# Performance work log

Hardware: AMD Instinct MI355X
Metric: run time of the kernel (lower is better)

## Reference

```python
import jax, jax.numpy as jnp
import numpy as np

NB, NA, NK, NC, NH, NW = 16, 5, 9, 13, 38, 38
MAXT = 50
NUM_LABELS = 2 * NK + 3  # class + 9 (x,y) keypoints + w + h
NOOBJ_SCALE, OBJ_SCALE = 1.0, 5.0
COORD_SCALE, CLASS_SCALE = 1.0, 1.0
SIL_THRESH = 0.6
PRETRAIN_EPOCHS = 15
TH, SHARP, IMW, IMH = 80.0, 2.0, 640.0, 480.0  # utils.corner_confidence defaults


def _corner_conf(dx, dy):
    # dx, dy: pixel-space keypoint deltas, last axis = keypoints
    dist = jnp.sqrt(dx * dx + dy * dy)
    denom = np.exp(SHARP) - 1.0
    c = jnp.where(dist < TH, (jnp.exp(SHARP * (1.0 - dist / TH)) - 1.0) / denom, 0.0)
    return c.mean(axis=-1)


def region_loss(output, target, anchors, epoch):
    nB, _, nH, nW = output.shape
    nA, nK, nC = NA, NK, NC
    out = output.reshape(nB, nA, 2 * nK + 1 + nC, nH, nW)
    x = out[:, :, 0:2 * nK:2]  # (nB,nA,nK,nH,nW)
    y = out[:, :, 1:2 * nK:2]
    x = x.at[:, :, 0].set(jax.nn.sigmoid(x[:, :, 0]))  # only keypoint 0 is sigmoided
    y = y.at[:, :, 0].set(jax.nn.sigmoid(y[:, :, 0]))
    conf = jax.nn.sigmoid(out[:, :, 2 * nK])  # (nB,nA,nH,nW)
    # cls: (nB*nA, nC, nH*nW).transpose(1,2) -> rows ordered (b,a,h,w)
    cls_logits = out[:, :, 2 * nK + 1:].transpose(0, 1, 3, 4, 2).reshape(-1, nC)

    # ---- decoded corners (detached in the original via .data) ----
    gx_grid = jnp.arange(nW, dtype=output.dtype)
    gy_grid = jnp.arange(nH, dtype=output.dtype)[:, None]
    px = jax.lax.stop_gradient((x + gx_grid) / nW)  # (nB,nA,nK,nH,nW)
    py = jax.lax.stop_gradient((y + gy_grid) / nH)
    nAnch = nA * nH * nW
    px_f = px.transpose(0, 1, 3, 4, 2).reshape(nB, nAnch, nK)  # (b, a*h*w, kp)
    py_f = py.transpose(0, 1, 3, 4, 2).reshape(nB, nAnch, nK)

    # ---- build_targets (all constants w.r.t. grads) ----
    tgt = jax.lax.stop_gradient(target).reshape(nB, MAXT, NUM_LABELS)
    gt_x = tgt[:, :, 1:1 + 2 * nK:2]  # (nB,T,nK)
    gt_y = tgt[:, :, 2:2 + 2 * nK:2]
    # loop breaks at first x0 == 0 -> validity is a cumulative product
    valid = jnp.cumprod((gt_x[:, :, 0] != 0).astype(output.dtype), axis=1)  # (nB,T)

    # pass 1: silence anchors already confident for some GT
    dx = (px_f[:, None] - gt_x[:, :, None]) * IMW  # (nB,T,nAnch,nK)
    dy = (py_f[:, None] - gt_y[:, :, None]) * IMH
    confs = _corner_conf(dx, dy) * valid[:, :, None]  # (nB,T,nAnch); invalid->0 == init
    cur_confs = confs.max(axis=1)  # (nB,nAnch)
    conf_mask_flat = jnp.where(cur_confs > SIL_THRESH, 0.0, NOOBJ_SCALE).reshape(-1)

    # pass 2: per-GT assignment
    gi0 = jnp.floor(gt_x[:, :, 0] * nW).astype(jnp.int32)  # (nB,T)
    gj0 = jnp.floor(gt_y[:, :, 0] * nH).astype(jnp.int32)
    gw = tgt[:, :, NUM_LABELS - 2] * nW
    gh = tgt[:, :, NUM_LABELS - 1] * nH
    anc = jax.lax.stop_gradient(anchors).reshape(nA, 2)
    aw, ah = anc[:, 0], anc[:, 1]
    # bbox_iou with both boxes centered at (0,0)
    uw = jnp.maximum(gw[..., None], aw)
    uh = jnp.maximum(gh[..., None], ah)
    cw = gw[..., None] + aw - uw
    ch = gh[..., None] + ah - uh
    carea = cw * ch
    uarea = gw[..., None] * gh[..., None] + aw * ah - carea
    iou = jnp.where((cw > 0) & (ch > 0), carea / uarea, 0.0)  # (nB,T,nA)
    best_n = jnp.argmax(iou, axis=-1)  # (nB,T)

    # faithful to the original bug: pred_box fetched with best_n == -1 (wraps)
    nPix = nH * nW
    pxa = px_f.reshape(nB * nAnch, nK)
    pya = py_f.reshape(nB * nAnch, nK)
    pidx = (jnp.arange(nB)[:, None] * nAnch - nPix + gj0 * nW + gi0) % (nB * nAnch)
    dxx = (gt_x - pxa[pidx]) * IMW  # (nB,T,nK)
    dyy = (gt_y - pya[pidx]) * IMH
    tconf_vals = _corner_conf(dxx, dyy)  # (nB,T)

    Ntot = nB * nA * nH * nW
    flat = ((jnp.arange(nB)[:, None] * nA + best_n) * nH + gj0) * nW + gi0
    flat = jnp.where(valid > 0, flat, Ntot).reshape(-1)  # invalid -> dummy slot

    coord_mask = jnp.zeros(Ntot + 1, output.dtype).at[flat].set(1.0)[:-1]
    cls_mask = coord_mask
    conf_mask = jnp.concatenate([conf_mask_flat, jnp.zeros(1, output.dtype)]).at[flat].set(OBJ_SCALE)[:-1]
    vx = (gt_x * nW - gi0[..., None].astype(output.dtype)).reshape(-1, nK)
    vy = (gt_y * nH - gj0[..., None].astype(output.dtype)).reshape(-1, nK)
    txs = jnp.zeros((Ntot + 1, nK), output.dtype).at[flat].set(vx)[:-1]
    tys = jnp.zeros((Ntot + 1, nK), output.dtype).at[flat].set(vy)[:-1]
    tconf = jnp.zeros(Ntot + 1, output.dtype).at[flat].set(tconf_vals.reshape(-1))[:-1]
    tcls = jnp.zeros(Ntot + 1, output.dtype).at[flat].set(tgt[:, :, 0].reshape(-1))[:-1]

    # ---- losses ----
    cm = coord_mask.reshape(nB, nA, nH, nW)[..., None]
    x_p = x.transpose(0, 1, 3, 4, 2)  # (nB,nA,nH,nW,nK)
    y_p = y.transpose(0, 1, 3, 4, 2)
    loss_x = COORD_SCALE * 0.5 * jnp.sum(((x_p - txs.reshape(nB, nA, nH, nW, nK)) * cm) ** 2)
    loss_y = COORD_SCALE * 0.5 * jnp.sum(((y_p - tys.reshape(nB, nA, nH, nW, nK)) * cm) ** 2)
    sqcm = jnp.sqrt(conf_mask).reshape(nB, nA, nH, nW)
    loss_conf = 0.5 * jnp.sum(((conf - tconf.reshape(nB, nA, nH, nW)) * sqcm) ** 2)
    labels = jnp.clip(tcls.astype(jnp.int32), 0, nC - 1)
    logp = jax.nn.log_softmax(cls_logits, axis=-1)
    ce = -jnp.take_along_axis(logp, labels[:, None], axis=-1)[:, 0]
    loss_cls = CLASS_SCALE * jnp.sum(cls_mask * ce)
    loss = loss_x + loss_y + loss_cls
    if epoch > PRETRAIN_EPOCHS:
        loss = loss + loss_conf
    return loss


def setup_inputs() -> dict:
    key = jax.random.key(0)
    k1, k2, k3, k4, k5 = jax.random.split(key, 5)
    output = jax.random.normal(k1, (NB, NA * (2 * NK + 1 + NC), NH, NW), jnp.float32)
    kp = jax.random.uniform(k2, (NB, MAXT, NK, 2), jnp.float32, 0.05, 0.95)
    wh = jax.random.uniform(k3, (NB, MAXT, 2), jnp.float32, 0.05, 0.5)
    cls = jax.random.randint(k4, (NB, MAXT), 0, NC).astype(jnp.float32)
    nvalid = jax.random.randint(k5, (NB,), 1, 9)
    valid = (jnp.arange(MAXT)[None, :] < nvalid[:, None]).astype(jnp.float32)
    tgt = jnp.concatenate([cls[..., None], kp.reshape(NB, MAXT, 2 * NK), wh], axis=-1)
    target = (tgt * valid[..., None]).reshape(NB, MAXT * NUM_LABELS)
    anchors = jnp.array([1.08, 1.19, 3.42, 4.41, 6.63, 11.38, 9.42, 5.11, 16.62, 10.52], jnp.float32)
    return {"output": output, "target": target, "anchors": anchors, "epoch": 20}


def reference(output, target, anchors, epoch):
    return region_loss(output, target, anchors, epoch)
```

## Files before the change

### kernel.cpp

```cpp
#include <hip/hip_runtime.h>
#include <math.h>

#define NB 16
#define NA 5
#define NK 9
#define NC 13
#define NH 38
#define NW 38
#define MAXT 50
#define NUM_LABELS 21
#define NPIX (NH*NW)
#define NANCH (NA*NPIX)
#define NTOT (NB*NANCH)
#define CHTOT (2*NK+1+NC)

#define TH_F 80.0f
#define SHARP_F 2.0f
#define IMW_F 640.0f
#define IMH_F 480.0f
#define SIL_F 0.6f
#define OBJ_SCALE_F 5.0f
#define NOOBJ_SCALE_F 1.0f
#define PRETRAIN_EPOCHS 15
#define INV_DENOM 0.15651764274966565f

__device__ __forceinline__ float sigmoidf(float v) {
    return 1.0f / (1.0f + __expf(-v));
}

__global__ void prep_kernel(const float* __restrict__ out,
                            const float* __restrict__ tgt,
                            const float* __restrict__ anchors,
                            float* __restrict__ tdata,
                            int* __restrict__ flatidx,
                            int* __restrict__ nvalid,
                            float* __restrict__ d_out)
{
    const int b = blockIdx.x;
    const int t = threadIdx.x;
    __shared__ int nv_s;
    if (t == 0) {
        int nv = 0;
        for (int tt = 0; tt < MAXT; tt++) {
            if (tgt[(long)b * MAXT * NUM_LABELS + tt * NUM_LABELS + 1] != 0.0f) nv++;
            else break;
        }
        nv_s = nv;
        nvalid[b] = nv;
        if (b == 0) d_out[0] = 0.0f;
    }
    __syncthreads();
    const int nv = nv_s;
    if (t >= MAXT) return;
    if (t >= nv) { flatidx[b * MAXT + t] = -1; return; }

    const float* tp = tgt + (long)b * MAXT * NUM_LABELS + t * NUM_LABELS;
    float gx[NK], gy[NK];
#pragma unroll
    for (int k = 0; k < NK; k++) {
        gx[k] = tp[1 + 2 * k];
        gy[k] = tp[2 + 2 * k];
    }
    const int gi0 = (int)floorf(gx[0] * (float)NW);
    const int gj0 = (int)floorf(gy[0] * (float)NH);
    const float gw = tp[NUM_LABELS - 2] * (float)NW;
    const float gh = tp[NUM_LABELS - 1] * (float)NH;

    int best_n = 0;
    float best_iou = -1.0f;
#pragma unroll
    for (int a = 0; a < NA; a++) {
        const float aw = anchors[2 * a], ah = anchors[2 * a + 1];
        const float uw = fmaxf(gw, aw), uh = fmaxf(gh, ah);
        const float cw = gw + aw - uw, ch = gh + ah - uh;
        const float carea = cw * ch;
        const float uarea = gw * gh + aw * ah - carea;
        const float iou = (cw > 0.0f && ch > 0.0f) ? (carea / uarea) : 0.0f;
        if (iou > best_iou) { best_iou = iou; best_n = a; }
    }

    long p = (long)b * NANCH - NPIX + gj0 * NW + gi0;
    p %= (long)NTOT;
    if (p < 0) p += NTOT;
    const int bb  = (int)(p / NANCH);
    const int rem = (int)(p % NANCH);
    const int aa  = rem / NPIX;
    const int pix = rem % NPIX;
    const int jj  = pix / NW;
    const int ii  = pix % NW;

    const long base2 = ((long)bb * NA + aa) * CHTOT * NPIX + pix;
    float ssum = 0.0f;
#pragma unroll
    for (int k = 0; k < NK; k++) {
        float xv = out[base2 + (2 * k) * NPIX];
        float yv = out[base2 + (2 * k + 1) * NPIX];
        if (k == 0) { xv = sigmoidf(xv); yv = sigmoidf(yv); }
        const float px = (xv + (float)ii) / (float)NW;
        const float py = (yv + (float)jj) / (float)NH;
        const float dx = (gx[k] - px) * IMW_F;
        const float dy = (gy[k] - py) * IMH_F;
        const float d = sqrtf(dx * dx + dy * dy);
        const float c = (d < TH_F)
            ? (__expf(SHARP_F * (1.0f - d / TH_F)) - 1.0f) * INV_DENOM : 0.0f;
        ssum += c;
    }
    const float tconf = ssum * (1.0f / (float)NK);

    float* td = tdata + (long)(b * MAXT + t) * 20;
#pragma unroll
    for (int k = 0; k < NK; k++) {
        td[k]      = gx[k] * (float)NW - (float)gi0;
        td[NK + k] = gy[k] * (float)NH - (float)gj0;
    }
    td[18] = tconf;
    td[19] = tp[0];
    flatidx[b * MAXT + t] = ((b * NA + best_n) * NH + gj0) * NW + gi0;
}

__global__ void __launch_bounds__(256)
region_loss_kernel(const float* __restrict__ out,
                   const float* __restrict__ tgt,
                   const float* __restrict__ tdata,
                   const int* __restrict__ flatidx,
                   const int* __restrict__ nvalid,
                   const int* __restrict__ epoch,
                   float* __restrict__ d_out)
{
    const int idx = blockIdx.x * blockDim.x + threadIdx.x;
    float loss = 0.0f;
    if (idx < NTOT) {
        const int b   = idx / NANCH;
        const int rem = idx % NANCH;
        const int a   = rem / NPIX;
        const int pix = rem % NPIX;
        const int j   = pix / NW;
        const int i   = pix % NW;

        const long base = ((long)b * NA + a) * CHTOT * NPIX + pix;

        float x[NK], y[NK], px[NK], py[NK];
#pragma unroll
        for (int k = 0; k < NK; k++) {
            float xv = out[base + (2 * k) * NPIX];
            float yv = out[base + (2 * k + 1) * NPIX];
            if (k == 0) { xv = sigmoidf(xv); yv = sigmoidf(yv); }
            x[k] = xv; y[k] = yv;
            px[k] = (xv + (float)i) / (float)NW;
            py[k] = (yv + (float)j) / (float)NH;
        }
        const float conf = sigmoidf(out[base + (2 * NK) * NPIX]);

        const int nv = nvalid[b];
        const int tbase = b * MAXT;
        float cur_conf = 0.0f;
        int wt = -1;
        for (int t = 0; t < nv; t++) {
            const float* tp = tgt + (long)b * MAXT * NUM_LABELS + t * NUM_LABELS;
            float s = 0.0f;
#pragma unroll
            for (int k = 0; k < NK; k++) {
                const float dx = (px[k] - tp[1 + 2 * k]) * IMW_F;
                const float dy = (py[k] - tp[2 + 2 * k]) * IMH_F;
                const float d = sqrtf(dx * dx + dy * dy);
                const float c = (d < TH_F)
                    ? (__expf(SHARP_F * (1.0f - d / TH_F)) - 1.0f) * INV_DENOM : 0.0f;
                s += c;
            }
            cur_conf = fmaxf(cur_conf, s * (1.0f / (float)NK));
            if (flatidx[tbase + t] == idx) wt = t;
        }

        float conf_mask = (cur_conf > SIL_F) ? 0.0f : NOOBJ_SCALE_F;
        float tconf_c = 0.0f;

        if (wt >= 0) {
            const float* td = tdata + (long)(tbase + wt) * 20;
            conf_mask = OBJ_SCALE_F;
            tconf_c = td[18];
            float lx = 0.0f, ly = 0.0f;
#pragma unroll
            for (int k = 0; k < NK; k++) {
                const float ex = x[k] - td[k];
                const float ey = y[k] - td[NK + k];
                lx += ex * ex;
                ly += ey * ey;
            }
            loss += 0.5f * (lx + ly);
            int label = (int)td[19];
            label = min(max(label, 0), NC - 1);
            float lg[NC];
            float m = -3.402823466e38f;
#pragma unroll
            for (int c = 0; c < NC; c++) {
                lg[c] = out[base + (2 * NK + 1 + c) * NPIX];
                m = fmaxf(m, lg[c]);
            }
            float se = 0.0f;
#pragma unroll
            for (int c = 0; c < NC; c++) se += __expf(lg[c] - m);
            const float lse = m + __logf(se);
            loss += (lse - lg[label]);
        }

        if (*epoch > PRETRAIN_EPOCHS) {
            const float d = conf - tconf_c;
            loss += 0.5f * conf_mask * d * d;
        }
    }

#pragma unroll
    for (int off = 32; off > 0; off >>= 1)
        loss += __shfl_down(loss, off);
    __shared__ float ssum[4];
    const int lane = threadIdx.x & 63;
    const int w = threadIdx.x >> 6;
    if (lane == 0) ssum[w] = loss;
    __syncthreads();
    if (threadIdx.x == 0) {
        atomicAdd(d_out, ssum[0] + ssum[1] + ssum[2] + ssum[3]);
    }
}

extern "C" void kernel_launch(void* const* d_in, const int* in_sizes, int n_in,
                              void* d_out, int out_size, void* d_ws, size_t ws_size,
                              hipStream_t stream) {
    const float* output  = (const float*)d_in[0];
    const float* target  = (const float*)d_in[1];
    const float* anchors = (const float*)d_in[2];
    const int*   epoch   = (const int*)d_in[3];
    float* outp = (float*)d_out;

    float* tdata  = (float*)d_ws;
    int*   flati  = (int*)((char*)d_ws + (size_t)NB * MAXT * 20 * sizeof(float));
    int*   nvalid = (int*)((char*)flati + (size_t)NB * MAXT * sizeof(int));

    prep_kernel<<<NB, 64, 0, stream>>>(output, target, anchors, tdata, flati, nvalid, outp);
    region_loss_kernel<<<(NTOT + 255) / 256, 256, 0, stream>>>(
        output, target, tdata, flati, nvalid, epoch, outp);
}
```

Measured before the change: 89.55 us.

## Fuse target prep into main loss kernel using shared-memory GT tables

Merges the prep kernel into the per-anchor loss kernel: each block builds per-GT tables (pre-scaled keypoints, target offsets, tconf, class, flat index) for up to two batches in shared memory, with valid count computed via ballot. The inner GT loop then reads shared memory instead of global target/workspace data, and divides become multiplies. This removes the inter-kernel dependency and workspace round-trip at the cost of redundant prep work per block and a memset launch.

```diff
diff --git a/kernel.cpp b/kernel.cpp
--- a/kernel.cpp
+++ b/kernel.cpp
@@ -28,106 +28,109 @@
     return 1.0f / (1.0f + __expf(-v));
 }
 
-__global__ void prep_kernel(const float* __restrict__ out,
-                            const float* __restrict__ tgt,
-                            const float* __restrict__ anchors,
-                            float* __restrict__ tdata,
-                            int* __restrict__ flatidx,
-                            int* __restrict__ nvalid,
-                            float* __restrict__ d_out)
+__device__ __forceinline__ float corner_c(float dx, float dy) {
+    const float d = sqrtf(dx * dx + dy * dy);
+    return (d < TH_F)
+        ? (__expf(SHARP_F * (1.0f - d * (1.0f / TH_F))) - 1.0f) * INV_DENOM
+        : 0.0f;
+}
+
+__global__ void __launch_bounds__(256)
+region_loss_fused(const float* __restrict__ out,
+                  const float* __restrict__ tgt,
+                  const float* __restrict__ anchors,
+                  const int* __restrict__ epoch,
+                  float* __restrict__ d_out)
 {
-    const int b = blockIdx.x;
-    const int t = threadIdx.x;
-    __shared__ int nv_s;
-    if (t == 0) {
-        int nv = 0;
-        for (int tt = 0; tt < MAXT; tt++) {
-            if (tgt[(long)b * MAXT * NUM_LABELS + tt * NUM_LABELS + 1] != 0.0f) nv++;
-            else break;
-        }
-        nv_s = nv;
-        nvalid[b] = nv;
-        if (b == 0) d_out[0] = 0.0f;
+    __shared__ float s_gx[2][MAXT][NK];
+    __shared__ float s_gy[2][MAXT][NK];
+    __shared__ float s_vx[2][MAXT][NK];
+    __shared__ float s_vy[2][MAXT][NK];
+    __shared__ float s_tconf[2][MAXT];
+    __shared__ float s_tcls[2][MAXT];
+    __shared__ int   s_flat[2][MAXT];
+    __shared__ int   s_nv[2];
+
+    const int tid  = threadIdx.x;
+    const int idx0 = blockIdx.x * 256;
+    const int b0   = idx0 / NANCH;
+    const int idxL = min(idx0 + 255, NTOT - 1);
+    const int b1   = idxL / NANCH;
+
+    int which = -1, t = 0;
+    if (tid < MAXT) { which = 0; t = tid; }
+    else if (b1 != b0 && tid >= 128 && tid < 128 + MAXT) { which = 1; t = tid - 128; }
+
+    if (which >= 0) {
+        const int bb = b0 + which;
+        const float* tp = tgt + (long)bb * MAXT * NUM_LABELS + t * NUM_LABELS;
+        const float gx0 = tp[1];
+        const unsigned long long mask = __ballot(gx0 != 0.0f);
+        const int nv = __ffsll((unsigned long long)(~mask)) - 1;
+        if (t == 0) s_nv[which] = nv;
+
+        if (t < nv) {
+            float gx[NK], gy[NK];
+#pragma unroll
+            for (int k = 0; k < NK; k++) {
+                gx[k] = tp[1 + 2 * k];
+                gy[k] = tp[2 + 2 * k];
+            }
+            const int gi0 = (int)floorf(gx[0] * (float)NW);
+            const int gj0 = (int)floorf(gy[0] * (float)NH);
+            const float gw = tp[NUM_LABELS - 2] * (float)NW;
+            const float gh = tp[NUM_LABELS - 1] * (float)NH;
+
+            int best_n = 0;
+            float best_iou = -1.0f;
+#pragma unroll
+            for (int a = 0; a < NA; a++) {
+                const float aw = anchors[2 * a], ah = anchors[2 * a + 1];
+                const float uw = fmaxf(gw, aw), uh = fmaxf(gh, ah);
+                const float cw = gw + aw - uw, ch = gh + ah - uh;
+                const float carea = cw * ch;
+                const float uarea = gw * gh + aw * ah - carea;
+                const float iou = (cw > 0.0f && ch > 0.0f) ? (carea / uarea) : 0.0f;
+                if (iou > best_iou) { best_iou = iou; best_n = a; }
+            }
+
+            long p = (long)bb * NANCH - NPIX + gj0 * NW + gi0;
+            p %= (long)NTOT;
+            if (p < 0) p += NTOT;
+            const int pb  = (int)(p / NANCH);
+            const int rem = (int)(p % NANCH);
+            const int pa  = rem / NPIX;
+            const int pix = rem % NPIX;
+            const int jj  = pix / NW;
+            const int ii  = pix % NW;
+
+            const long base2 = ((long)pb * NA + pa) * CHTOT * NPIX + pix;
+            float ssum = 0.0f;
+#pragma unroll
+            for (int k = 0; k < NK; k++) {
+                float xv = out[base2 + (2 * k) * NPIX];
+                float yv = out[base2 + (2 * k + 1) * NPIX];
+                if (k == 0) { xv = sigmoidf(xv); yv = sigmoidf(yv); }
+                const float px = (xv + (float)ii) * (1.0f / (float)NW);
+                const float py = (yv + (float)jj) * (1.0f / (float)NH);
+                ssum += corner_c((gx[k] - px) * IMW_F, (gy[k] - py) * IMH_F);
+            }
+
+#pragma unroll
+            for (int k = 0; k < NK; k++) {
+                s_gx[which][t][k] = gx[k] * IMW_F;
+                s_gy[which][t][k] = gy[k] * IMH_F;
+                s_vx[which][t][k] = gx[k] * (float)NW - (float)gi0;
+                s_vy[which][t][k] = gy[k] * (float)NH - (float)gj0;
+            }
+            s_tconf[which][t] = ssum * (1.0f / (float)NK);
+            s_tcls[which][t]  = tp[0];
+            s_flat[which][t]  = ((bb * NA + best_n) * NH + gj0) * NW + gi0;
+        }
     }
     __syncthreads();
-    const int nv = nv_s;
-    if (t >= MAXT) return;
-    if (t >= nv) { flatidx[b * MAXT + t] = -1; return; }
-
-    const float* tp = tgt + (long)b * MAXT * NUM_LABELS + t * NUM_LABELS;
-    float gx[NK], gy[NK];
-#pragma unroll
-    for (int k = 0; k < NK; k++) {
-        gx[k] = tp[1 + 2 * k];
-        gy[k] = tp[2 + 2 * k];
-    }
-    const int gi0 = (int)floorf(gx[0] * (float)NW);
-    const int gj0 = (int)floorf(gy[0] * (float)NH);
-    const float gw = tp[NUM_LABELS - 2] * (float)NW;
-    const float gh = tp[NUM_LABELS - 1] * (float)NH;
-
-    int best_n = 0;
-    float best_iou = -1.0f;
-#pragma unroll
-    for (int a = 0; a < NA; a++) {
-        const float aw = anchors[2 * a], ah = anchors[2 * a + 1];
-        const float uw = fmaxf(gw, aw), uh = fmaxf(gh, ah);
-        const float cw = gw + aw - uw, ch = gh + ah - uh;
-        const float carea = cw * ch;
-        const float uarea = gw * gh + aw * ah - carea;
-        const float iou = (cw > 0.0f && ch > 0.0f) ? (carea / uarea) : 0.0f;
-        if (iou > best_iou) { best_iou = iou; best_n = a; }
-    }
-
-    long p = (long)b * NANCH - NPIX + gj0 * NW + gi0;
-    p %= (long)NTOT;
-    if (p < 0) p += NTOT;
-    const int bb  = (int)(p / NANCH);
-    const int rem = (int)(p % NANCH);
-    const int aa  = rem / NPIX;
-    const int pix = rem % NPIX;
-    const int jj  = pix / NW;
-    const int ii  = pix % NW;
-
-    const long base2 = ((long)bb * NA + aa) * CHTOT * NPIX + pix;
-    float ssum = 0.0f;
-#pragma unroll
-    for (int k = 0; k < NK; k++) {
-        float xv = out[base2 + (2 * k) * NPIX];
-        float yv = out[base2 + (2 * k + 1) * NPIX];
-        if (k == 0) { xv = sigmoidf(xv); yv = sigmoidf(yv); }
-        const float px = (xv + (float)ii) / (float)NW;
-        const float py = (yv + (float)jj) / (float)NH;
-        const float dx = (gx[k] - px) * IMW_F;
-        const float dy = (gy[k] - py) * IMH_F;
-        const float d = sqrtf(dx * dx + dy * dy);
-        const float c = (d < TH_F)
-            ? (__expf(SHARP_F * (1.0f - d / TH_F)) - 1.0f) * INV_DENOM : 0.0f;
-        ssum += c;
-    }
-    const float tconf = ssum * (1.0f / (float)NK);
-
-    float* td = tdata + (long)(b * MAXT + t) * 20;
-#pragma unroll
-    for (int k = 0; k < NK; k++) {
-        td[k]      = gx[k] * (float)NW - (float)gi0;
-        td[NK + k] = gy[k] * (float)NH - (float)gj0;
-    }
-    td[18] = tconf;
-    td[19] = tp[0];
-    flatidx[b * MAXT + t] = ((b * NA + best_n) * NH + gj0) * NW + gi0;
-}
-
-__global__ void __launch_bounds__(256)
-region_loss_kernel(const float* __restrict__ out,
-                   const float* __restrict__ tgt,
-                   const float* __restrict__ tdata,
-                   const int* __restrict__ flatidx,
-                   const int* __restrict__ nvalid,
-                   const int* __restrict__ epoch,
-                   float* __restrict__ d_out)
-{
-    const int idx = blockIdx.x * blockDim.x + threadIdx.x;
+
+    const int idx = idx0 + tid;
     float loss = 0.0f;
     if (idx < NTOT) {
         const int b   = idx / NANCH;
@@ -136,58 +139,51 @@
         const int pix = rem % NPIX;
         const int j   = pix / NW;
         const int i   = pix % NW;
+        const int w2  = (b == b0) ? 0 : 1;
 
         const long base = ((long)b * NA + a) * CHTOT * NPIX + pix;
 
-        float x[NK], y[NK], px[NK], py[NK];
+        float x[NK], y[NK], pxw[NK], pyw[NK];
 #pragma unroll
         for (int k = 0; k < NK; k++) {
             float xv = out[base + (2 * k) * NPIX];
             float yv = out[base + (2 * k + 1) * NPIX];
             if (k == 0) { xv = sigmoidf(xv); yv = sigmoidf(yv); }
             x[k] = xv; y[k] = yv;
-            px[k] = (xv + (float)i) / (float)NW;
-            py[k] = (yv + (float)j) / (float)NH;
+            pxw[k] = (xv + (float)i) * (IMW_F / (float)NW);
+            pyw[k] = (yv + (float)j) * (IMH_F / (float)NH);
         }
         const float conf = sigmoidf(out[base + (2 * NK) * NPIX]);
 
-        const int nv = nvalid[b];
-        const int tbase = b * MAXT;
+        const int nv = s_nv[w2];
         float cur_conf = 0.0f;
         int wt = -1;
         for (int t = 0; t < nv; t++) {
-            const float* tp = tgt + (long)b * MAXT * NUM_LABELS + t * NUM_LABELS;
             float s = 0.0f;
 #pragma unroll
             for (int k = 0; k < NK; k++) {
-                const float dx = (px[k] - tp[1 + 2 * k]) * IMW_F;
-                const float dy = (py[k] - tp[2 + 2 * k]) * IMH_F;
-                const float d = sqrtf(dx * dx + dy * dy);
-                const float c = (d < TH_F)
-                    ? (__expf(SHARP_F * (1.0f - d / TH_F)) - 1.0f) * INV_DENOM : 0.0f;
-                s += c;
+                s += corner_c(pxw[k] - s_gx[w2][t][k], pyw[k] - s_gy[w2][t][k]);
             }
             cur_conf = fmaxf(cur_conf, s * (1.0f / (float)NK));
-            if (flatidx[tbase + t] == idx) wt = t;
+            if (s_flat[w2][t] == idx) wt = t;
         }
 
         float conf_mask = (cur_conf > SIL_F) ? 0.0f : NOOBJ_SCALE_F;
         float tconf_c = 0.0f;
 
         if (wt >= 0) {
-            const float* td = tdata + (long)(tbase + wt) * 20;
             conf_mask = OBJ_SCALE_F;
-            tconf_c = td[18];
+            tconf_c = s_tconf[w2][wt];
             float lx = 0.0f, ly = 0.0f;
 #pragma unroll
             for (int k = 0; k < NK; k++) {
-                const float ex = x[k] - td[k];
-                const float ey = y[k] - td[NK + k];
+                const float ex = x[k] - s_vx[w2][wt][k];
+                const float ey = y[k] - s_vy[w2][wt][k];
                 lx += ex * ex;
                 ly += ey * ey;
             }
             loss += 0.5f * (lx + ly);
-            int label = (int)td[19];
+            int label = (int)s_tcls[w2][wt];
             label = min(max(label, 0), NC - 1);
             float lg[NC];
             float m = -3.402823466e38f;
@@ -199,8 +195,7 @@
             float se = 0.0f;
 #pragma unroll
             for (int c = 0; c < NC; c++) se += __expf(lg[c] - m);
-            const float lse = m + __logf(se);
-            loss += (lse - lg[label]);
+            loss += (m + __logf(se)) - lg[label];
         }
 
         if (*epoch > PRETRAIN_EPOCHS) {
@@ -213,11 +208,11 @@
     for (int off = 32; off > 0; off >>= 1)
         loss += __shfl_down(loss, off);
     __shared__ float ssum[4];
-    const int lane = threadIdx.x & 63;
-    const int w = threadIdx.x >> 6;
+    const int lane = tid & 63;
+    const int w = tid >> 6;
     if (lane == 0) ssum[w] = loss;
     __syncthreads();
-    if (threadIdx.x == 0) {
+    if (tid == 0) {
         atomicAdd(d_out, ssum[0] + ssum[1] + ssum[2] + ssum[3]);
     }
 }
@@ -231,11 +226,8 @@
     const int*   epoch   = (const int*)d_in[3];
     float* outp = (float*)d_out;
 
-    float* tdata  = (float*)d_ws;
-    int*   flati  = (int*)((char*)d_ws + (size_t)NB * MAXT * 20 * sizeof(float));
-    int*   nvalid = (int*)((char*)flati + (size_t)NB * MAXT * sizeof(int));
-
-    prep_kernel<<<NB, 64, 0, stream>>>(output, target, anchors, tdata, flati, nvalid, outp);
-    region_loss_kernel<<<(NTOT + 255) / 256, 256, 0, stream>>>(
-        output, target, tdata, flati, nvalid, epoch, outp);
-}
+    (void)d_ws; (void)ws_size;
+    hipMemsetAsync(outp, 0, sizeof(float), stream);
+    region_loss_fused<<<(NTOT + 255) / 256, 256, 0, stream>>>(
+        output, target, anchors, epoch, outp);
+}
```

Result: faster. 78.11 us (-12.8%).
